# Kernel tuning notes

Hardware: AMD Instinct MI355X
Metric: run time of the kernel (lower is better)

Reference implementation:

```python
import jax, jax.numpy as jnp
import numpy as np

MD = 4  # max displacement -> 9x9 = 81 window, matches the +8 pad and 81 output channels


def setup_inputs() -> dict:
    key = jax.random.key(0)
    k1, k2 = jax.random.split(key)
    first = jax.random.normal(k1, (8, 256, 96, 128), dtype=jnp.float32)
    second = jax.random.normal(k2, (8, 256, 96, 128), dtype=jnp.float32)
    return {"first": first, "second": second}


def reference(first, second):
    # first, second: [B, C, H, W]
    B, C, H, W = first.shape
    # pad second spatially by MD on each side (the rbot1 [B, H+8, W+8, C] buffer)
    pad = jnp.pad(second, ((0, 0), (0, 0), (MD, MD), (MD, MD)))
    outs = []
    # channel ordering matches CUDA kernel: top_channel = (dy+4)*9 + (dx+4)
    for dy in range(2 * MD + 1):
        for dx in range(2 * MD + 1):
            shifted = jax.lax.dynamic_slice(pad, (0, 0, dy, dx), (B, C, H, W))
            outs.append(jnp.einsum('bchw,bchw->bhw', first, shifted))
    # kernel divides the per-pixel dot product by the channel count
    return jnp.stack(outs, axis=1) / C  # [B, 81, H, W]
```

## Files before the change

### kernel.cpp

```cpp
#include <hip/hip_runtime.h>

namespace {
constexpr int Bn = 8, Cn = 256, Hn = 96, Wn = 128;
constexpr int HWn = Hn * Wn;
constexpr int CHWn = Cn * HWn;
constexpr int ND = 9;
constexpr int TILESH = Hn / 4;
constexpr int NBLK = Bn * TILESH * ND;
constexpr int PERX = NBLK / 8;
}

__device__ __forceinline__ float dpp_shr1(float x) {
  return __int_as_float(__builtin_amdgcn_update_dpp(
      0, __float_as_int(x), 0x111 , 0xF, 0xF, true));
}
__device__ __forceinline__ float dpp_shl1(float x) {
  return __int_as_float(__builtin_amdgcn_update_dpp(
      0, __float_as_int(x), 0x101 , 0xF, 0xF, true));
}

struct Ch {
  float4 sa, sb, fa, fb;
};

__global__ __launch_bounds__(64, 2) void corr_kernel(
    const float* __restrict__ first, const float* __restrict__ second,
    float* __restrict__ out)
{
  const int lane = threadIdx.x;
  const int bid = blockIdx.x;
  const int logical = (bid & 7) * PERX + (bid >> 3);
  const int dy = logical % ND;
  const int t = logical / ND;
  const int b = t / TILESH;
  const int h0 = (t % TILESH) * 4;

  const int hs = lane >> 4;
  const int w0 = (lane & 15) << 3;

  const int gr = h0 + hs + dy - 4;
  const float m = (gr >= 0 && gr < Hn) ? 1.0f : 0.0f;
  const int cg = min(max(gr, 0), Hn - 1);

  const float* ssrc = second + b * CHWn + cg * Wn + w0;
  const float* fsrc = first + b * CHWn + (h0 + hs) * Wn + w0;

  float acc[ND][8];
#pragma unroll
  for (int dx = 0; dx < ND; ++dx)
#pragma unroll
    for (int p = 0; p < 8; ++p) acc[dx][p] = 0.f;

  auto LOADCH = [&](int coff) -> Ch {
    Ch r;
    r.sa = *(const float4*)(ssrc + coff);
    r.sb = *(const float4*)(ssrc + coff + 4);
    r.fa = *(const float4*)(fsrc + coff);
    r.fb = *(const float4*)(fsrc + coff + 4);
    return r;
  };

  auto COMP = [&](const Ch& ch) {
    const float sa0 = ch.sa.x * m, sa1 = ch.sa.y * m, sa2 = ch.sa.z * m, sa3 = ch.sa.w * m;
    const float sb0 = ch.sb.x * m, sb1 = ch.sb.y * m, sb2 = ch.sb.z * m, sb3 = ch.sb.w * m;
    const float s[16] = {
        dpp_shr1(sb0), dpp_shr1(sb1), dpp_shr1(sb2), dpp_shr1(sb3),
        sa0, sa1, sa2, sa3,
        sb0, sb1, sb2, sb3,
        dpp_shl1(sa0), dpp_shl1(sa1), dpp_shl1(sa2), dpp_shl1(sa3)};
    const float f[8] = {ch.fa.x, ch.fa.y, ch.fa.z, ch.fa.w,
                        ch.fb.x, ch.fb.y, ch.fb.z, ch.fb.w};
#pragma unroll
    for (int dx = 0; dx < ND; ++dx)
#pragma unroll
      for (int p = 0; p < 8; ++p)
        acc[dx][p] = fmaf(f[p], s[p + dx], acc[dx][p]);
  };

  Ch L0 = LOADCH(0);
  Ch L1 = LOADCH(HWn);
  int coff = 2 * HWn;
#pragma unroll 1
  for (int it = 0; it < (Cn - 2) / 2; ++it) {
    Ch N0 = LOADCH(coff);
    Ch N1 = LOADCH(coff + HWn);
    COMP(L0);
    COMP(L1);
    L0 = N0;
    L1 = N1;
    coff += 2 * HWn;
  }
  COMP(L0);
  COMP(L1);

  const float sc = 1.0f / Cn;
  float* obase = out + ((b * 81 + dy * ND) * Hn + (h0 + hs)) * Wn + w0;
#pragma unroll
  for (int dx = 0; dx < ND; ++dx) {
    float4 o0 = make_float4(acc[dx][0] * sc, acc[dx][1] * sc,
                            acc[dx][2] * sc, acc[dx][3] * sc);
    float4 o1 = make_float4(acc[dx][4] * sc, acc[dx][5] * sc,
                            acc[dx][6] * sc, acc[dx][7] * sc);
    *(float4*)(obase + dx * HWn) = o0;
    *(float4*)(obase + dx * HWn + 4) = o1;
  }
}

extern "C" void kernel_launch(void* const* d_in, const int* in_sizes, int n_in,
                              void* d_out, int out_size, void* d_ws, size_t ws_size,
                              hipStream_t stream) {
  const float* first = (const float*)d_in[0];
  const float* second = (const float*)d_in[1];
  float* out = (float*)d_out;
  corr_kernel<<<dim3(NBLK), dim3(64), 0, stream>>>(first, second, out);
}
```

Measured before the change: 98.27 us.

## Split channel reduction across two waves with LDS reduction of accumulators

```diff
diff --git a/kernel.cpp b/kernel.cpp
--- a/kernel.cpp
+++ b/kernel.cpp
@@ -8,6 +8,8 @@
 constexpr int TILESH = Hn / 4;
 constexpr int NBLK = Bn * TILESH * ND;
 constexpr int PERX = NBLK / 8;
+constexpr int NW = 2;
+constexpr int CPW = Cn / NW;
 }
 
 __device__ __forceinline__ float dpp_shr1(float x) {
@@ -23,11 +25,15 @@
   float4 sa, sb, fa, fb;
 };
 
-__global__ __launch_bounds__(64, 2) void corr_kernel(
+__global__ __launch_bounds__(128) void corr_kernel(
     const float* __restrict__ first, const float* __restrict__ second,
     float* __restrict__ out)
 {
-  const int lane = threadIdx.x;
+  __shared__ float red[ND][8][64];
+
+  const int tid = threadIdx.x;
+  const int wv = tid >> 6;
+  const int lane = tid & 63;
   const int bid = blockIdx.x;
   const int logical = (bid & 7) * PERX + (bid >> 3);
   const int dy = logical % ND;
@@ -42,8 +48,8 @@
   const float m = (gr >= 0 && gr < Hn) ? 1.0f : 0.0f;
   const int cg = min(max(gr, 0), Hn - 1);
 
-  const float* ssrc = second + b * CHWn + cg * Wn + w0;
-  const float* fsrc = first + b * CHWn + (h0 + hs) * Wn + w0;
+  const float* ssrc = second + b * CHWn + wv * CPW * HWn + cg * Wn + w0;
+  const float* fsrc = first + b * CHWn + wv * CPW * HWn + (h0 + hs) * Wn + w0;
 
   float acc[ND][8];
 #pragma unroll
@@ -61,13 +67,11 @@
   };
 
   auto COMP = [&](const Ch& ch) {
-    const float sa0 = ch.sa.x * m, sa1 = ch.sa.y * m, sa2 = ch.sa.z * m, sa3 = ch.sa.w * m;
-    const float sb0 = ch.sb.x * m, sb1 = ch.sb.y * m, sb2 = ch.sb.z * m, sb3 = ch.sb.w * m;
     const float s[16] = {
-        dpp_shr1(sb0), dpp_shr1(sb1), dpp_shr1(sb2), dpp_shr1(sb3),
-        sa0, sa1, sa2, sa3,
-        sb0, sb1, sb2, sb3,
-        dpp_shl1(sa0), dpp_shl1(sa1), dpp_shl1(sa2), dpp_shl1(sa3)};
+        dpp_shr1(ch.sb.x), dpp_shr1(ch.sb.y), dpp_shr1(ch.sb.z), dpp_shr1(ch.sb.w),
+        ch.sa.x, ch.sa.y, ch.sa.z, ch.sa.w,
+        ch.sb.x, ch.sb.y, ch.sb.z, ch.sb.w,
+        dpp_shl1(ch.sa.x), dpp_shl1(ch.sa.y), dpp_shl1(ch.sa.z), dpp_shl1(ch.sa.w)};
     const float f[8] = {ch.fa.x, ch.fa.y, ch.fa.z, ch.fa.w,
                         ch.fb.x, ch.fb.y, ch.fb.z, ch.fb.w};
 #pragma unroll
@@ -81,7 +85,7 @@
   Ch L1 = LOADCH(HWn);
   int coff = 2 * HWn;
 #pragma unroll 1
-  for (int it = 0; it < (Cn - 2) / 2; ++it) {
+  for (int it = 0; it < (CPW - 2) / 2; ++it) {
     Ch N0 = LOADCH(coff);
     Ch N1 = LOADCH(coff + HWn);
     COMP(L0);
@@ -93,16 +97,38 @@
   COMP(L0);
   COMP(L1);
 
-  const float sc = 1.0f / Cn;
+  const float scale = m * (1.0f / Cn);
   float* obase = out + ((b * 81 + dy * ND) * Hn + (h0 + hs)) * Wn + w0;
+
+  if (wv == 0) {
+#pragma unroll
+    for (int dx = 5; dx < ND; ++dx)
+#pragma unroll
+      for (int p = 0; p < 8; ++p) red[dx][p][lane] = acc[dx][p];
+  } else {
+#pragma unroll
+    for (int dx = 0; dx < 5; ++dx)
+#pragma unroll
+      for (int p = 0; p < 8; ++p) red[dx][p][lane] = acc[dx][p];
+  }
+  __syncthreads();
+
+  const int dlo = (wv == 0) ? 0 : 5;
+  const int dhi = (wv == 0) ? 5 : ND;
 #pragma unroll
   for (int dx = 0; dx < ND; ++dx) {
-    float4 o0 = make_float4(acc[dx][0] * sc, acc[dx][1] * sc,
-                            acc[dx][2] * sc, acc[dx][3] * sc);
-    float4 o1 = make_float4(acc[dx][4] * sc, acc[dx][5] * sc,
-                            acc[dx][6] * sc, acc[dx][7] * sc);
-    *(float4*)(obase + dx * HWn) = o0;
-    *(float4*)(obase + dx * HWn + 4) = o1;
+    if (dx >= dlo && dx < dhi) {
+      float4 o0 = make_float4((acc[dx][0] + red[dx][0][lane]) * scale,
+                              (acc[dx][1] + red[dx][1][lane]) * scale,
+                              (acc[dx][2] + red[dx][2][lane]) * scale,
+                              (acc[dx][3] + red[dx][3][lane]) * scale);
+      float4 o1 = make_float4((acc[dx][4] + red[dx][4][lane]) * scale,
+                              (acc[dx][5] + red[dx][5][lane]) * scale,
+                              (acc[dx][6] + red[dx][6][lane]) * scale,
+                              (acc[dx][7] + red[dx][7][lane]) * scale);
+      *(float4*)(obase + dx * HWn) = o0;
+      *(float4*)(obase + dx * HWn + 4) = o1;
+    }
   }
 }
 
@@ -112,5 +138,5 @@
   const float* first = (const float*)d_in[0];
   const float* second = (const float*)d_in[1];
   float* out = (float*)d_out;
-  corr_kernel<<<dim3(NBLK), dim3(64), 0, stream>>>(first, second, out);
+  corr_kernel<<<dim3(NBLK), dim3(NW * 64), 0, stream>>>(first, second, out);
 }
```

Result: slower. 112.7 us (+14.7%).

## Split channel reduction across wave halves and halve rows per block

Applied to the files above, without the earlier changes.

```diff
diff --git a/kernel.cpp b/kernel.cpp
--- a/kernel.cpp
+++ b/kernel.cpp
@@ -5,9 +5,10 @@
 constexpr int HWn = Hn * Wn;
 constexpr int CHWn = Cn * HWn;
 constexpr int ND = 9;
-constexpr int TILESH = Hn / 4;
+constexpr int TILESH = Hn / 2;
 constexpr int NBLK = Bn * TILESH * ND;
 constexpr int PERX = NBLK / 8;
+constexpr int CHALF = Cn / 2;
 }
 
 __device__ __forceinline__ float dpp_shr1(float x) {
@@ -23,7 +24,7 @@
   float4 sa, sb, fa, fb;
 };
 
-__global__ __launch_bounds__(64, 2) void corr_kernel(
+__global__ __launch_bounds__(64) void corr_kernel(
     const float* __restrict__ first, const float* __restrict__ second,
     float* __restrict__ out)
 {
@@ -33,17 +34,18 @@
   const int dy = logical % ND;
   const int t = logical / ND;
   const int b = t / TILESH;
-  const int h0 = (t % TILESH) * 4;
+  const int h0 = (t % TILESH) * 2;
 
-  const int hs = lane >> 4;
+  const int hs = (lane >> 4) & 1;
+  const int chalf = lane >> 5;
   const int w0 = (lane & 15) << 3;
 
   const int gr = h0 + hs + dy - 4;
   const float m = (gr >= 0 && gr < Hn) ? 1.0f : 0.0f;
   const int cg = min(max(gr, 0), Hn - 1);
 
-  const float* ssrc = second + b * CHWn + cg * Wn + w0;
-  const float* fsrc = first + b * CHWn + (h0 + hs) * Wn + w0;
+  const float* ssrc = second + b * CHWn + chalf * CHALF * HWn + cg * Wn + w0;
+  const float* fsrc = first + b * CHWn + chalf * CHALF * HWn + (h0 + hs) * Wn + w0;
 
   float acc[ND][8];
 #pragma unroll
@@ -61,13 +63,11 @@
   };
 
   auto COMP = [&](const Ch& ch) {
-    const float sa0 = ch.sa.x * m, sa1 = ch.sa.y * m, sa2 = ch.sa.z * m, sa3 = ch.sa.w * m;
-    const float sb0 = ch.sb.x * m, sb1 = ch.sb.y * m, sb2 = ch.sb.z * m, sb3 = ch.sb.w * m;
     const float s[16] = {
-        dpp_shr1(sb0), dpp_shr1(sb1), dpp_shr1(sb2), dpp_shr1(sb3),
-        sa0, sa1, sa2, sa3,
-        sb0, sb1, sb2, sb3,
-        dpp_shl1(sa0), dpp_shl1(sa1), dpp_shl1(sa2), dpp_shl1(sa3)};
+        dpp_shr1(ch.sb.x), dpp_shr1(ch.sb.y), dpp_shr1(ch.sb.z), dpp_shr1(ch.sb.w),
+        ch.sa.x, ch.sa.y, ch.sa.z, ch.sa.w,
+        ch.sb.x, ch.sb.y, ch.sb.z, ch.sb.w,
+        dpp_shl1(ch.sa.x), dpp_shl1(ch.sa.y), dpp_shl1(ch.sa.z), dpp_shl1(ch.sa.w)};
     const float f[8] = {ch.fa.x, ch.fa.y, ch.fa.z, ch.fa.w,
                         ch.fb.x, ch.fb.y, ch.fb.z, ch.fb.w};
 #pragma unroll
@@ -81,7 +81,7 @@
   Ch L1 = LOADCH(HWn);
   int coff = 2 * HWn;
 #pragma unroll 1
-  for (int it = 0; it < (Cn - 2) / 2; ++it) {
+  for (int it = 0; it < (CHALF - 2) / 2; ++it) {
     Ch N0 = LOADCH(coff);
     Ch N1 = LOADCH(coff + HWn);
     COMP(L0);
@@ -93,16 +93,35 @@
   COMP(L0);
   COMP(L1);
 
-  const float sc = 1.0f / Cn;
+#pragma unroll
+  for (int dx = 0; dx < ND; ++dx)
+#pragma unroll
+    for (int p = 0; p < 8; ++p)
+      acc[dx][p] += __shfl_xor(acc[dx][p], 32);
+
+  const float scale = m * (1.0f / Cn);
   float* obase = out + ((b * 81 + dy * ND) * Hn + (h0 + hs)) * Wn + w0;
+
+  if (lane < 32) {
 #pragma unroll
-  for (int dx = 0; dx < ND; ++dx) {
-    float4 o0 = make_float4(acc[dx][0] * sc, acc[dx][1] * sc,
-                            acc[dx][2] * sc, acc[dx][3] * sc);
-    float4 o1 = make_float4(acc[dx][4] * sc, acc[dx][5] * sc,
-                            acc[dx][6] * sc, acc[dx][7] * sc);
-    *(float4*)(obase + dx * HWn) = o0;
-    *(float4*)(obase + dx * HWn + 4) = o1;
+    for (int dx = 0; dx < 5; ++dx) {
+      float4 o0 = make_float4(acc[dx][0] * scale, acc[dx][1] * scale,
+                              acc[dx][2] * scale, acc[dx][3] * scale);
+      float4 o1 = make_float4(acc[dx][4] * scale, acc[dx][5] * scale,
+                              acc[dx][6] * scale, acc[dx][7] * scale);
+      *(float4*)(obase + dx * HWn) = o0;
+      *(float4*)(obase + dx * HWn + 4) = o1;
+    }
+  } else {
+#pragma unroll
+    for (int dx = 5; dx < ND; ++dx) {
+      float4 o0 = make_float4(acc[dx][0] * scale, acc[dx][1] * scale,
+                              acc[dx][2] * scale, acc[dx][3] * scale);
+      float4 o1 = make_float4(acc[dx][4] * scale, acc[dx][5] * scale,
+                              acc[dx][6] * scale, acc[dx][7] * scale);
+      *(float4*)(obase + dx * HWn) = o0;
+      *(float4*)(obase + dx * HWn + 4) = o1;
+    }
   }
 }
 
```

Result: slower. 116.4 us (+18.4%).

## Prepack inputs to fp16 pairs and compute correlation with dot2 via LDS tiles

Applied to the files above, without the earlier changes.

```diff
diff --git a/kernel.cpp b/kernel.cpp
--- a/kernel.cpp
+++ b/kernel.cpp
@@ -1,56 +1,207 @@
 #include <hip/hip_runtime.h>
+
+typedef _Float16 half2v __attribute__((ext_vector_type(2)));
 
 namespace {
 constexpr int Bn = 8, Cn = 256, Hn = 96, Wn = 128;
 constexpr int HWn = Hn * Wn;
 constexpr int CHWn = Cn * HWn;
+constexpr int CPn = Cn / 2;
 constexpr int ND = 9;
-constexpr int TILESH = Hn / 4;
-constexpr int NBLK = Bn * TILESH * ND;
-constexpr int PERX = NBLK / 8;
-}
-
-__device__ __forceinline__ float dpp_shr1(float x) {
-  return __int_as_float(__builtin_amdgcn_update_dpp(
-      0, __float_as_int(x), 0x111 , 0xF, 0xF, true));
-}
-__device__ __forceinline__ float dpp_shl1(float x) {
-  return __int_as_float(__builtin_amdgcn_update_dpp(
-      0, __float_as_int(x), 0x101 , 0xF, 0xF, true));
-}
-
-struct Ch {
-  float4 sa, sb, fa, fb;
-};
-
-__global__ __launch_bounds__(64, 2) void corr_kernel(
+constexpr int TH = 4;
+constexpr int HQ = Hn / TH;
+constexpr int NBLK = Bn * HQ;
+constexpr size_t WSF_U32 = (size_t)Bn * CPn * HWn;
+constexpr size_t WS_NEED = 2 * WSF_U32 * 4;
+constexpr int ROWP = 132;
+constexpr int STEPSZ = 16 * ROWP;
+}
+
+__device__ __forceinline__ unsigned dpp_shr1(unsigned x) {
+  return (unsigned)__builtin_amdgcn_update_dpp(0, (int)x, 0x111, 0xF, 0xF, true);
+}
+__device__ __forceinline__ unsigned dpp_shl1(unsigned x) {
+  return (unsigned)__builtin_amdgcn_update_dpp(0, (int)x, 0x101, 0xF, 0xF, true);
+}
+
+__device__ __forceinline__ float dot2h(unsigned a, unsigned b, float c) {
+#if __has_builtin(__builtin_amdgcn_fdot2)
+  return __builtin_amdgcn_fdot2(__builtin_bit_cast(half2v, a),
+                                __builtin_bit_cast(half2v, b), c, false);
+#else
+  float d;
+  asm("v_dot2_f32_f16 %0, %1, %2, %3" : "=v"(d) : "v"(a), "v"(b), "v"(c));
+  return d;
+#endif
+}
+
+__global__ __launch_bounds__(256) void prepack(
+    const float* __restrict__ fin, const float* __restrict__ sin_,
+    unsigned* __restrict__ wf, unsigned* __restrict__ wsp)
+{
+  const int total = Bn * CPn * Hn * (Wn / 4);
+  for (int q = blockIdx.x * blockDim.x + threadIdx.x; q < total;
+       q += gridDim.x * blockDim.x) {
+    const int w4 = q & 31;
+    const int h = (q >> 5) % Hn;
+    const int bcp = q / (32 * Hn);
+    const int b = bcp >> 7, cp = bcp & 127;
+    const int i0 = ((b * Cn + 2 * cp) * Hn + h) * Wn + w4 * 4;
+    float4 fa = *(const float4*)(fin + i0);
+    float4 fb = *(const float4*)(fin + i0 + HWn);
+    float4 sa = *(const float4*)(sin_ + i0);
+    float4 sb = *(const float4*)(sin_ + i0 + HWn);
+    uint4 pf, ps;
+    pf.x = __builtin_bit_cast(unsigned, __builtin_amdgcn_cvt_pkrtz(fa.x, fb.x));
+    pf.y = __builtin_bit_cast(unsigned, __builtin_amdgcn_cvt_pkrtz(fa.y, fb.y));
+    pf.z = __builtin_bit_cast(unsigned, __builtin_amdgcn_cvt_pkrtz(fa.z, fb.z));
+    pf.w = __builtin_bit_cast(unsigned, __builtin_amdgcn_cvt_pkrtz(fa.w, fb.w));
+    ps.x = __builtin_bit_cast(unsigned, __builtin_amdgcn_cvt_pkrtz(sa.x, sb.x));
+    ps.y = __builtin_bit_cast(unsigned, __builtin_amdgcn_cvt_pkrtz(sa.y, sb.y));
+    ps.z = __builtin_bit_cast(unsigned, __builtin_amdgcn_cvt_pkrtz(sa.z, sb.z));
+    ps.w = __builtin_bit_cast(unsigned, __builtin_amdgcn_cvt_pkrtz(sa.w, sb.w));
+    *(uint4*)(wf + (size_t)q * 4) = pf;
+    *(uint4*)(wsp + (size_t)q * 4) = ps;
+  }
+}
+
+__global__ __launch_bounds__(576) void corr_dot2(
+    const unsigned* __restrict__ wf, const unsigned* __restrict__ wsp,
+    float* __restrict__ out)
+{
+  __shared__ __align__(16) unsigned LB[2][2 * STEPSZ];
+
+  const int tid = threadIdx.x;
+  const int dy = tid >> 6;
+  const int lane = tid & 63;
+  const int hs = (lane >> 4) & 3;
+  const int w0 = (lane & 15) << 3;
+
+  const int bid = blockIdx.x;
+  const int logical = (bid & 7) * (NBLK / 8) + (bid >> 3);
+  const int b = logical / HQ;
+  const int h0 = (logical % HQ) * TH;
+
+  const int t0 = tid, t1 = tid + 576;
+
+  float acc[ND][8];
+#pragma unroll
+  for (int dx = 0; dx < ND; ++dx)
+#pragma unroll
+    for (int p = 0; p < 8; ++p) acc[dx][p] = 0.f;
+
+  uint4 stg0, stg1;
+  auto LOADT = [&](int t, int k, uint4& v) {
+    const int step = t >> 9;
+    const int r = (t >> 5) & 15;
+    const int li = t & 31;
+    const int cp = 2 * k + step;
+    if (r < 12) {
+      const int grow = h0 - 4 + r;
+      if (grow >= 0 && grow < Hn)
+        v = *(const uint4*)(wsp + ((size_t)(b * CPn + cp) * Hn + grow) * Wn + li * 4);
+      else
+        v = make_uint4(0, 0, 0, 0);
+    } else {
+      const int hr = h0 + (r - 12);
+      v = *(const uint4*)(wf + ((size_t)(b * CPn + cp) * Hn + hr) * Wn + li * 4);
+    }
+  };
+  auto LOADS = [&](int k) {
+    LOADT(t0, k, stg0);
+    if (t1 < 1024) LOADT(t1, k, stg1);
+  };
+  auto WRITET = [&](int t, unsigned* lb, const uint4& v) {
+    const int step = t >> 9;
+    const int r = (t >> 5) & 15;
+    const int li = t & 31;
+    *(uint4*)(lb + step * STEPSZ + r * ROWP + li * 4) = v;
+  };
+  auto WRITES = [&](unsigned* lb) {
+    WRITET(t0, lb, stg0);
+    if (t1 < 1024) WRITET(t1, lb, stg1);
+  };
+
+  auto COMPUTE = [&](const unsigned* lb) {
+#pragma unroll
+    for (int step = 0; step < 2; ++step) {
+      const unsigned* base = lb + step * STEPSZ;
+      const unsigned* srow = base + (hs + dy) * ROWP + w0;
+      const unsigned* frow = base + (12 + hs) * ROWP + w0;
+      uint4 sA = *(const uint4*)(srow);
+      uint4 sB = *(const uint4*)(srow + 4);
+      uint4 fA = *(const uint4*)(frow);
+      uint4 fB = *(const uint4*)(frow + 4);
+      const unsigned o0 = sA.x, o1 = sA.y, o2 = sA.z, o3 = sA.w;
+      const unsigned o4 = sB.x, o5 = sB.y, o6 = sB.z, o7 = sB.w;
+      const unsigned sw[16] = {
+          dpp_shr1(o4), dpp_shr1(o5), dpp_shr1(o6), dpp_shr1(o7),
+          o0, o1, o2, o3, o4, o5, o6, o7,
+          dpp_shl1(o0), dpp_shl1(o1), dpp_shl1(o2), dpp_shl1(o3)};
+      const unsigned fv[8] = {fA.x, fA.y, fA.z, fA.w, fB.x, fB.y, fB.z, fB.w};
+#pragma unroll
+      for (int dx = 0; dx < ND; ++dx)
+#pragma unroll
+        for (int p = 0; p < 8; ++p)
+          acc[dx][p] = dot2h(fv[p], sw[p + dx], acc[dx][p]);
+    }
+  };
+
+  LOADS(0);
+  WRITES(&LB[0][0]);
+  __syncthreads();
+#pragma unroll 1
+  for (int k = 0; k < CPn / 2; ++k) {
+    if (k < CPn / 2 - 1) LOADS(k + 1);
+    COMPUTE(&LB[k & 1][0]);
+    if (k < CPn / 2 - 1) WRITES(&LB[(k + 1) & 1][0]);
+    __syncthreads();
+  }
+
+  const float sc = 1.0f / Cn;
+  float* obase = out + ((size_t)(b * 81 + dy * ND) * Hn + (h0 + hs)) * Wn + w0;
+#pragma unroll
+  for (int dx = 0; dx < ND; ++dx) {
+    float4 q0 = make_float4(acc[dx][0] * sc, acc[dx][1] * sc,
+                            acc[dx][2] * sc, acc[dx][3] * sc);
+    float4 q1 = make_float4(acc[dx][4] * sc, acc[dx][5] * sc,
+                            acc[dx][6] * sc, acc[dx][7] * sc);
+    *(float4*)(obase + (size_t)dx * HWn) = q0;
+    *(float4*)(obase + (size_t)dx * HWn + 4) = q1;
+  }
+}
+
+__device__ __forceinline__ float fdpp_shr1(float x) {
+  return __int_as_float(__builtin_amdgcn_update_dpp(0, __float_as_int(x), 0x111, 0xF, 0xF, true));
+}
+__device__ __forceinline__ float fdpp_shl1(float x) {
+  return __int_as_float(__builtin_amdgcn_update_dpp(0, __float_as_int(x), 0x101, 0xF, 0xF, true));
+}
+struct Ch { float4 sa, sb, fa, fb; };
+
+__global__ __launch_bounds__(64) void corr_r2(
     const float* __restrict__ first, const float* __restrict__ second,
     float* __restrict__ out)
 {
   const int lane = threadIdx.x;
   const int bid = blockIdx.x;
-  const int logical = (bid & 7) * PERX + (bid >> 3);
+  const int logical = (bid & 7) * 216 + (bid >> 3);
   const int dy = logical % ND;
   const int t = logical / ND;
-  const int b = t / TILESH;
-  const int h0 = (t % TILESH) * 4;
-
+  const int b = t / 24;
+  const int h0 = (t % 24) * 4;
   const int hs = lane >> 4;
   const int w0 = (lane & 15) << 3;
-
   const int gr = h0 + hs + dy - 4;
   const float m = (gr >= 0 && gr < Hn) ? 1.0f : 0.0f;
   const int cg = min(max(gr, 0), Hn - 1);
-
   const float* ssrc = second + b * CHWn + cg * Wn + w0;
   const float* fsrc = first + b * CHWn + (h0 + hs) * Wn + w0;
-
   float acc[ND][8];
 #pragma unroll
   for (int dx = 0; dx < ND; ++dx)
 #pragma unroll
     for (int p = 0; p < 8; ++p) acc[dx][p] = 0.f;
-
   auto LOADCH = [&](int coff) -> Ch {
     Ch r;
     r.sa = *(const float4*)(ssrc + coff);
@@ -59,24 +210,19 @@
     r.fb = *(const float4*)(fsrc + coff + 4);
     return r;
   };
-
   auto COMP = [&](const Ch& ch) {
     const float sa0 = ch.sa.x * m, sa1 = ch.sa.y * m, sa2 = ch.sa.z * m, sa3 = ch.sa.w * m;
     const float sb0 = ch.sb.x * m, sb1 = ch.sb.y * m, sb2 = ch.sb.z * m, sb3 = ch.sb.w * m;
-    const float s[16] = {
-        dpp_shr1(sb0), dpp_shr1(sb1), dpp_shr1(sb2), dpp_shr1(sb3),
-        sa0, sa1, sa2, sa3,
-        sb0, sb1, sb2, sb3,
-        dpp_shl1(sa0), dpp_shl1(sa1), dpp_shl1(sa2), dpp_shl1(sa3)};
+    const float s[16] = {fdpp_shr1(sb0), fdpp_shr1(sb1), fdpp_shr1(sb2), fdpp_shr1(sb3),
+                         sa0, sa1, sa2, sa3, sb0, sb1, sb2, sb3,
+                         fdpp_shl1(sa0), fdpp_shl1(sa1), fdpp_shl1(sa2), fdpp_shl1(sa3)};
     const float f[8] = {ch.fa.x, ch.fa.y, ch.fa.z, ch.fa.w,
                         ch.fb.x, ch.fb.y, ch.fb.z, ch.fb.w};
 #pragma unroll
     for (int dx = 0; dx < ND; ++dx)
 #pragma unroll
-      for (int p = 0; p < 8; ++p)
-        acc[dx][p] = fmaf(f[p], s[p + dx], acc[dx][p]);
-  };
-
+      for (int p = 0; p < 8; ++p) acc[dx][p] = fmaf(f[p], s[p + dx], acc[dx][p]);
+  };
   Ch L0 = LOADCH(0);
   Ch L1 = LOADCH(HWn);
   int coff = 2 * HWn;
@@ -84,23 +230,17 @@
   for (int it = 0; it < (Cn - 2) / 2; ++it) {
     Ch N0 = LOADCH(coff);
     Ch N1 = LOADCH(coff + HWn);
-    COMP(L0);
-    COMP(L1);
-    L0 = N0;
-    L1 = N1;
+    COMP(L0); COMP(L1);
+    L0 = N0; L1 = N1;
     coff += 2 * HWn;
   }
-  COMP(L0);
-  COMP(L1);
-
+  COMP(L0); COMP(L1);
   const float sc = 1.0f / Cn;
   float* obase = out + ((b * 81 + dy * ND) * Hn + (h0 + hs)) * Wn + w0;
 #pragma unroll
   for (int dx = 0; dx < ND; ++dx) {
-    float4 o0 = make_float4(acc[dx][0] * sc, acc[dx][1] * sc,
-                            acc[dx][2] * sc, acc[dx][3] * sc);
-    float4 o1 = make_float4(acc[dx][4] * sc, acc[dx][5] * sc,
-                            acc[dx][6] * sc, acc[dx][7] * sc);
+    float4 o0 = make_float4(acc[dx][0] * sc, acc[dx][1] * sc, acc[dx][2] * sc, acc[dx][3] * sc);
+    float4 o1 = make_float4(acc[dx][4] * sc, acc[dx][5] * sc, acc[dx][6] * sc, acc[dx][7] * sc);
     *(float4*)(obase + dx * HWn) = o0;
     *(float4*)(obase + dx * HWn + 4) = o1;
   }
@@ -112,5 +252,12 @@
   const float* first = (const float*)d_in[0];
   const float* second = (const float*)d_in[1];
   float* out = (float*)d_out;
-  corr_kernel<<<dim3(NBLK), dim3(64), 0, stream>>>(first, second, out);
-}
+  if (ws_size >= WS_NEED) {
+    unsigned* wf = (unsigned*)d_ws;
+    unsigned* wsp = wf + WSF_U32;
+    prepack<<<dim3(2048), dim3(256), 0, stream>>>(first, second, wf, wsp);
+    corr_dot2<<<dim3(NBLK), dim3(576), 0, stream>>>(wf, wsp, out);
+  } else {
+    corr_r2<<<dim3(1728), dim3(64), 0, stream>>>(first, second, out);
+  }
+}
```

After: 138.6 us. 1.41x slower.
